# Kernel optimization log

Measured on AMD Instinct MI355X. Metric: run time of the kernel, lower is better.

## Reference

```python
import jax, jax.numpy as jnp
import numpy as np
import math

B, S, D, H, L, DF = 16, 512, 512, 8, 6, 2048
DK = D // H
EPS = 1e-6


def _xavier(key, shape):
    # xavier_uniform over the last two dims (matches nn.init.xavier_uniform_)
    fan_in, fan_out = shape[-2], shape[-1]
    lim = math.sqrt(6.0 / (fan_in + fan_out))
    return jax.random.uniform(key, shape, jnp.float32, -lim, lim)


def setup_inputs() -> dict:
    key = jax.random.key(0)
    ks = jax.random.split(key, 12)
    return {
        "x": jax.random.normal(ks[0], (B, S, D), jnp.float32),
        "pe_table": jax.random.normal(ks[1], (S, D), jnp.float32),  # _4by8_pe weight
        "pe_q_w": _xavier(ks[2], (D, D)), "pe_q_b": jnp.zeros((D,), jnp.float32),
        "pe_k_w": _xavier(ks[3], (D, D)), "pe_k_b": jnp.zeros((D,), jnp.float32),
        "Wq": _xavier(ks[4], (L, D, D)), "bq": jnp.zeros((L, D), jnp.float32),
        "Wk": _xavier(ks[5], (L, D, D)), "bk": jnp.zeros((L, D), jnp.float32),
        "Wv": _xavier(ks[6], (L, D, D)), "bv": jnp.zeros((L, D), jnp.float32),
        "Wo": _xavier(ks[7], (L, D, D)), "bo": jnp.zeros((L, D), jnp.float32),
        "ln1_g": jnp.ones((L, D), jnp.float32), "ln1_b": jnp.zeros((L, D), jnp.float32),
        "W1": _xavier(ks[8], (L, D, DF)), "b1": jnp.zeros((L, DF), jnp.float32),
        "W2": _xavier(ks[9], (L, DF, D)), "b2": jnp.zeros((L, D), jnp.float32),
        "ln2_g": jnp.ones((L, D), jnp.float32), "ln2_b": jnp.zeros((L, D), jnp.float32),
    }


def _layernorm(y, g, b):
    m = jnp.mean(y, axis=-1, keepdims=True)
    v = jnp.var(y, axis=-1, keepdims=True)  # biased, as torch LayerNorm
    return (y - m) * jax.lax.rsqrt(v + EPS) * g + b


def reference(x, pe_table, pe_q_w, pe_q_b, pe_k_w, pe_k_b,
              Wq, bq, Wk, bk, Wv, bv, Wo, bo,
              ln1_g, ln1_b, W1, b1, W2, b2, ln2_g, ln2_b):
    scale = math.sqrt(2 * DK)
    h = x * math.sqrt(D)

    # scores_pe is identical for every batch element (pe_onehot = arange repeated)
    pq = (pe_table @ pe_q_w + pe_q_b).reshape(S, H, DK).transpose(1, 0, 2)  # [H,S,dk]
    pk = (pe_table @ pe_k_w + pe_k_b).reshape(S, H, DK).transpose(1, 0, 2)  # [H,S,dk]
    scores_pe = jnp.einsum('hqd,hkd->hqk', pq, pk) / scale  # [H,S,S]

    def step(h, p):
        wq, bq_, wk, bk_, wv, bv_, wo, bo_, g1, gb1, w1, fb1, w2, fb2, g2, gb2 = p
        q = (h @ wq + bq_).reshape(B, S, H, DK).transpose(0, 2, 1, 3)  # [B,H,S,dk]
        k = (h @ wk + bk_).reshape(B, S, H, DK).transpose(0, 2, 1, 3)
        v = (h @ wv + bv_).reshape(B, S, H, DK).transpose(0, 2, 1, 3)
        scores = jnp.einsum('bhqd,bhkd->bhqk', q, k) / scale + scores_pe  # [B,H,S,S]
        attn = jax.nn.softmax(scores, axis=-1)
        o = jnp.einsum('bhqk,bhkd->bhqd', attn, v).transpose(0, 2, 1, 3).reshape(B, S, D)
        o = o @ wo + bo_
        h1 = _layernorm(o + h, g1, gb1)
        f = jax.nn.gelu(h1 @ w1 + fb1, approximate=False) @ w2 + fb2
        h2 = _layernorm(f + h1, g2, gb2)
        return h2, None

    params = (Wq, bq, Wk, bk, Wv, bv, Wo, bo, ln1_g, ln1_b, W1, b1, W2, b2, ln2_g, ln2_b)
    h, _ = jax.lax.scan(step, h, params)
    pe_out = jnp.broadcast_to(pe_table, (B, S, D))
    return h, pe_out
```

## Files before the change

kernel.cpp:

```cpp
#include <hip/hip_runtime.h>
#include <hip/hip_bf16.h>

typedef __hip_bfloat16 bf16;
typedef short bf16x8 __attribute__((ext_vector_type(8)));
typedef float f32x4 __attribute__((ext_vector_type(4)));

#define DEV static __device__ __forceinline__

DEV f32x4 fzero4(){ f32x4 z; z[0]=0.f; z[1]=0.f; z[2]=0.f; z[3]=0.f; return z; }

DEV void gl2lds16(const bf16* g, bf16* l){
  __builtin_amdgcn_global_load_lds(
    (const __attribute__((address_space(1))) void*)g,
    (__attribute__((address_space(3))) void*)l, 16, 0, 0);
}

enum { EP_F32=0, EP_BF16=1, EP_GELU=2, EP_HILO=3, EP_QKV=4 };

template<int EPI, int NMT>
__global__ __launch_bounds__(256) void gemm_bt(
    const bf16* A0, const bf16* A1, const bf16* A2,
    const bf16* B0, const bf16* B1, const bf16* B2,
    int npass, int lda, int ldb, int M, int N, int K,
    const float* __restrict__ bs0, const float* __restrict__ bs1, const float* __restrict__ bs2,
    float alpha, void* o0, void* o1, void* o2,
    int azs, int bzs, int ozs)
{
  constexpr int BM = NMT*32;
  __shared__ __align__(16) bf16 As[BM*32];
  __shared__ __align__(16) bf16 Bs[128*32];
  const int t = threadIdx.x;
  const int lane = t & 63;
  const int w = t >> 6;
  const int wr = w >> 1, wc = w & 1;
  const int m0 = blockIdx.y * BM, n0 = blockIdx.x * 128;
  const int l15 = lane & 15, l4 = lane >> 4;
  const int grow = (lane >> 2);
  const int gcol = (lane & 3) * 8;
  const int z = blockIdx.z;
  if (azs){ A0 += (size_t)z*azs; if(A1) A1 += (size_t)z*azs; if(A2) A2 += (size_t)z*azs; }
  if (bzs){ B0 += (size_t)z*bzs; if(B1) B1 += (size_t)z*bzs; if(B2) B2 += (size_t)z*bzs; }

  f32x4 acc[NMT][4];
  #pragma unroll
  for (int i=0;i<NMT;i++)
    #pragma unroll
    for (int j=0;j<4;j++) acc[i][j] = fzero4();

  for (int p=0;p<npass;p++){
    const bf16* Ag = (p==0) ? A0 : ((p==1) ? A1 : A2);
    const bf16* Bg = (p==0) ? B0 : ((p==1) ? B1 : B2);
    for (int k0=0;k0<K;k0+=32){
      if constexpr (NMT==4){
        #pragma unroll
        for (int q=0;q<2;q++){
          int row = w*32 + q*16 + grow;
          gl2lds16(Ag + (size_t)(m0+row)*lda + k0 + gcol, As + (w*32+q*16)*32);
          gl2lds16(Bg + (size_t)(n0+row)*ldb + k0 + gcol, Bs + (w*32+q*16)*32);
        }
      } else {
        int rA = w*16 + grow;
        gl2lds16(Ag + (size_t)(m0+rA)*lda + k0 + gcol, As + w*16*32);
        #pragma unroll
        for (int sb=0;sb<2;sb++){
          int rB = (2*w+sb)*16 + grow;
          gl2lds16(Bg + (size_t)(n0+rB)*ldb + k0 + gcol, Bs + (2*w+sb)*16*32);
        }
      }
      __syncthreads();
      bf16x8 af[NMT], bfv[4];
      #pragma unroll
      for (int mt=0;mt<NMT;mt++) af[mt] = *(const bf16x8*)(As + (wr*(NMT*16)+mt*16+l15)*32 + 8*l4);
      #pragma unroll
      for (int nt=0;nt<4;nt++) bfv[nt] = *(const bf16x8*)(Bs + (wc*64+nt*16+l15)*32 + 8*l4);
      #pragma unroll
      for (int mt=0;mt<NMT;mt++)
        #pragma unroll
        for (int nt=0;nt<4;nt++)
          acc[mt][nt] = __builtin_amdgcn_mfma_f32_16x16x32_bf16(af[mt], bfv[nt], acc[mt][nt], 0, 0, 0);
      __syncthreads();
    }
  }

  #pragma unroll
  for (int mt=0;mt<NMT;mt++){
    #pragma unroll
    for (int nt=0;nt<4;nt++){
      const int crow = m0 + wr*(NMT*16) + mt*16 + l4*4;
      const int ccol = n0 + wc*64 + nt*16 + l15;
      #pragma unroll
      for (int j=0;j<4;j++){
        float v = acc[mt][nt][j];
        int r = crow + j;
        if (EPI==EP_F32){
          float b = bs0 ? bs0[ccol] : 0.f;
          ((float*)o0)[(size_t)r*N + ccol] = alpha*v + b;
        } else if (EPI==EP_BF16){
          float b = bs0 ? bs0[ccol] : 0.f;
          ((bf16*)o0 + (size_t)z*ozs)[(size_t)r*N + ccol] = __float2bfloat16(alpha*v + b);
        } else if (EPI==EP_GELU){
          float xx = v + bs0[ccol];
          float g = 0.5f*xx*(1.f + erff(xx*0.70710678118654752f));
          ((bf16*)o0)[(size_t)r*N + ccol] = __float2bfloat16(g);
        } else if (EPI==EP_HILO){
          float xx = v + bs0[ccol];
          bf16 hi = __float2bfloat16(xx);
          ((bf16*)o0)[(size_t)r*N + ccol] = hi;
          ((bf16*)o1)[(size_t)r*N + ccol] = __float2bfloat16(xx - __bfloat162float(hi));
        } else {
          int n = ccol;
          if (n < 512){
            ((bf16*)o0)[(size_t)r*512 + n] = __float2bfloat16(v + bs0[n]);
          } else if (n < 1024){
            ((bf16*)o1)[(size_t)r*512 + (n-512)] = __float2bfloat16(v + bs1[n-512]);
          } else {
            int d = n - 1024;
            int bb = r >> 9, s = r & 511;
            int hh = d >> 6, dd = d & 63;
            ((bf16*)o2)[(size_t)(((bb*8)+hh)*64 + dd)*512 + s] = __float2bfloat16(v + bs2[d]);
          }
        }
      }
    }
  }
}

template<int SPLIT>
__global__ __launch_bounds__(256) void attn_mfma(
  const bf16* __restrict__ Q, const bf16* __restrict__ Qlo,
  const bf16* __restrict__ Kh, const bf16* __restrict__ Klo,
  const bf16* __restrict__ VT, const bf16* __restrict__ SPE,
  bf16* __restrict__ O)
{
  __shared__ __align__(16) bf16 K_lds[64*64];
  __shared__ __align__(16) bf16 V_lds[64*64];
  __shared__ __align__(16) bf16 Klo_lds[SPLIT ? 64*64 : 8];
  __shared__ __align__(16) bf16 P_lds[4][16*64];
  const int t = threadIdx.x;
  const int lane = t & 63, w = t >> 6;
  const int l15 = lane & 15, l4 = lane >> 4;
  const int bid = blockIdx.x;
  const int h = bid & 7;
  const int s2 = bid >> 3;
  const int b = s2 >> 3, qblk = s2 & 7;
  const int q0 = qblk*64 + w*16;
  const float inv_scale = 0.08838834764831845f;
  const int xorv = (l15 & 7) << 3;

  bf16x8 qf[2], qflo[2];
  #pragma unroll
  for (int kst=0;kst<2;kst++){
    qf[kst] = *(const bf16x8*)(Q + (size_t)(b*512 + q0 + l15)*512 + h*64 + kst*32 + 8*l4);
    if (SPLIT) qflo[kst] = *(const bf16x8*)(Qlo + (size_t)(b*512 + q0 + l15)*512 + h*64 + kst*32 + 8*l4);
  }
  f32x4 accO[4];
  #pragma unroll
  for (int dt=0;dt<4;dt++) accO[dt] = fzero4();
  float mrow[4], lrow[4];
  #pragma unroll
  for (int j=0;j<4;j++){ mrow[j] = -1e30f; lrow[j] = 0.f; }

  const bf16* spe_h = SPE + (size_t)h*262144;
  const bf16* vbase = VT + (size_t)((b*8)+h)*32768;

  for (int n0=0;n0<512;n0+=64){
    #pragma unroll
    for (int st=0;st<2;st++){
      int rl = w*16 + st*8 + (lane>>3);
      int jj = (lane&7) ^ (rl&7);
      gl2lds16(Kh + (size_t)(b*512 + n0 + rl)*512 + h*64 + jj*8, K_lds + (w*16+st*8)*64);
      if (SPLIT)
        gl2lds16(Klo + (size_t)(b*512 + n0 + rl)*512 + h*64 + jj*8, Klo_lds + (w*16+st*8)*64);
      gl2lds16(vbase + (size_t)rl*512 + n0 + jj*8, V_lds + (w*16+st*8)*64);
    }
    __syncthreads();

    f32x4 sc[4];
    #pragma unroll
    for (int c=0;c<4;c++) sc[c] = fzero4();
    #pragma unroll
    for (int c=0;c<4;c++){
      const int rr = c*16 + l15;
      #pragma unroll
      for (int kst=0;kst<2;kst++){
        bf16x8 kf = *(const bf16x8*)(K_lds + rr*64 + ((kst*32 + 8*l4) ^ xorv));
        sc[c] = __builtin_amdgcn_mfma_f32_16x16x32_bf16(qf[kst], kf, sc[c], 0,0,0);
        if (SPLIT){
          sc[c] = __builtin_amdgcn_mfma_f32_16x16x32_bf16(qflo[kst], kf, sc[c], 0,0,0);
          bf16x8 kfl = *(const bf16x8*)(Klo_lds + rr*64 + ((kst*32 + 8*l4) ^ xorv));
          sc[c] = __builtin_amdgcn_mfma_f32_16x16x32_bf16(qf[kst], kfl, sc[c], 0,0,0);
        }
      }
    }
    float sv[4][4];
    #pragma unroll
    for (int c=0;c<4;c++)
      #pragma unroll
      for (int j=0;j<4;j++){
        int qr = q0 + l4*4 + j;
        sv[c][j] = sc[c][j]*inv_scale + __bfloat162float(spe_h[(size_t)qr*512 + n0 + c*16 + l15]);
      }
    float fac[4];
    #pragma unroll
    for (int j=0;j<4;j++){
      float m2 = fmaxf(fmaxf(sv[0][j],sv[1][j]), fmaxf(sv[2][j],sv[3][j]));
      m2 = fmaxf(m2, __shfl_xor(m2,1));
      m2 = fmaxf(m2, __shfl_xor(m2,2));
      m2 = fmaxf(m2, __shfl_xor(m2,4));
      m2 = fmaxf(m2, __shfl_xor(m2,8));
      float mn = fmaxf(mrow[j], m2);
      fac[j] = __expf(mrow[j] - mn);
      mrow[j] = mn;
    }
    #pragma unroll
    for (int j=0;j<4;j++){
      int row = l4*4 + j;
      float ts = 0.f;
      #pragma unroll
      for (int c=0;c<4;c++){
        float pv = __expf(sv[c][j] - mrow[j]);
        ts += pv;
        P_lds[w][row*64 + ((c*16 + l15) ^ ((row&7)<<3))] = __float2bfloat16(pv);
      }
      ts += __shfl_xor(ts,1); ts += __shfl_xor(ts,2);
      ts += __shfl_xor(ts,4); ts += __shfl_xor(ts,8);
      lrow[j] = lrow[j]*fac[j] + ts;
      #pragma unroll
      for (int dt=0;dt<4;dt++) accO[dt][j] *= fac[j];
    }
    #pragma unroll
    for (int kv=0;kv<2;kv++){
      bf16x8 pf = *(const bf16x8*)(P_lds[w] + l15*64 + ((kv*32 + 8*l4) ^ xorv));
      #pragma unroll
      for (int dt=0;dt<4;dt++){
        const int d = dt*16 + l15;
        bf16x8 vf = *(const bf16x8*)(V_lds + d*64 + ((kv*32 + 8*l4) ^ xorv));
        accO[dt] = __builtin_amdgcn_mfma_f32_16x16x32_bf16(pf, vf, accO[dt], 0,0,0);
      }
    }
    __syncthreads();
  }
  #pragma unroll
  for (int dt=0;dt<4;dt++)
    #pragma unroll
    for (int j=0;j<4;j++){
      float v = accO[dt][j] / lrow[j];
      int r = q0 + l4*4 + j;
      O[(size_t)(b*512+r)*512 + h*64 + dt*16 + l15] = __float2bfloat16(v);
    }
}

__global__ __launch_bounds__(256) void ln_kernel(
  const float* __restrict__ tmp, const float* __restrict__ resid,
  const float* __restrict__ g, const float* __restrict__ bta,
  float* __restrict__ outf, bf16* __restrict__ outb)
{
  const int row = blockIdx.x*4 + (threadIdx.x>>6);
  const int lane = threadIdx.x & 63;
  const size_t base = (size_t)row*512 + lane*8;
  float4 a0 = *(const float4*)(tmp+base),   a1 = *(const float4*)(tmp+base+4);
  float4 r0 = *(const float4*)(resid+base), r1 = *(const float4*)(resid+base+4);
  float x[8];
  x[0]=a0.x+r0.x; x[1]=a0.y+r0.y; x[2]=a0.z+r0.z; x[3]=a0.w+r0.w;
  x[4]=a1.x+r1.x; x[5]=a1.y+r1.y; x[6]=a1.z+r1.z; x[7]=a1.w+r1.w;
  float s=0.f, sq=0.f;
  #pragma unroll
  for (int i=0;i<8;i++){ s += x[i]; sq += x[i]*x[i]; }
  #pragma unroll
  for (int d=1; d<64; d<<=1){ s += __shfl_xor(s,d); sq += __shfl_xor(sq,d); }
  float mean = s*(1.f/512.f);
  float var = sq*(1.f/512.f) - mean*mean;
  float rr = rsqrtf(var + 1e-6f);
  #pragma unroll
  for (int i=0;i<8;i++){
    int d = lane*8 + i;
    float y = (x[i]-mean)*rr*g[d] + bta[d];
    outf[base+i] = y;
    outb[base+i] = __float2bfloat16(y);
  }
}

template<bool LO>
__global__ __launch_bounds__(256) void tcast(
  const float* __restrict__ src, int srcStride,
  bf16* __restrict__ dst, int dstStride, bf16* __restrict__ dlo,
  int R, int C)
{
  __shared__ float tile[32][33];
  const int z = blockIdx.z;
  src += (size_t)z*srcStride;
  dst += (size_t)z*dstStride;
  const int tx = threadIdx.x & 31, ty = threadIdx.x >> 5;
  const int r0 = blockIdx.y*32, c0 = blockIdx.x*32;
  #pragma unroll
  for (int p=0;p<4;p++)
    tile[ty+8*p][tx] = src[(size_t)(r0+ty+8*p)*C + c0+tx];
  __syncthreads();
  #pragma unroll
  for (int p=0;p<4;p++){
    float v = tile[tx][ty+8*p];
    bf16 hi = __float2bfloat16(v);
    dst[(size_t)(c0+ty+8*p)*R + r0+tx] = hi;
    if (LO) dlo[(size_t)(c0+ty+8*p)*R + r0+tx] = __float2bfloat16(v - __bfloat162float(hi));
  }
}

__global__ void castbf(const float* __restrict__ in, bf16* __restrict__ out, int n){
  int i = blockIdx.x*blockDim.x + threadIdx.x;
  if (i < n) out[i] = __float2bfloat16(in[i]);
}

__global__ void init_h(const float* __restrict__ x, float* __restrict__ hf,
                       bf16* __restrict__ hb, bf16* __restrict__ hlo, int n){
  int i = blockIdx.x*blockDim.x + threadIdx.x;
  if (i < n){
    float v = x[i]*22.627416997969522f;
    hf[i] = v;
    bf16 hi = __float2bfloat16(v);
    hb[i] = hi;
    hlo[i] = __float2bfloat16(v - __bfloat162float(hi));
  }
}

__global__ void write_out(const float* __restrict__ hf, const float* __restrict__ pe,
                          float* __restrict__ out, int n1){
  int i = blockIdx.x*blockDim.x + threadIdx.x;
  if (i < n1){
    out[i] = hf[i];
    out[n1 + i] = pe[i & 262143];
  }
}

extern "C" void kernel_launch(void* const* d_in, const int* in_sizes, int n_in,
                              void* d_out, int out_size, void* d_ws, size_t ws_size,
                              hipStream_t stream)
{
  const float* x    = (const float*)d_in[0];
  const float* pe   = (const float*)d_in[1];
  const float* peqw = (const float*)d_in[2];
  const float* peqb = (const float*)d_in[3];
  const float* pekw = (const float*)d_in[4];
  const float* pekb = (const float*)d_in[5];
  const float* Wq   = (const float*)d_in[6];
  const float* bq   = (const float*)d_in[7];
  const float* Wk   = (const float*)d_in[8];
  const float* bk   = (const float*)d_in[9];
  const float* Wv   = (const float*)d_in[10];
  const float* bv   = (const float*)d_in[11];
  const float* Wo   = (const float*)d_in[12];
  const float* bo   = (const float*)d_in[13];
  const float* g1   = (const float*)d_in[14];
  const float* bb1  = (const float*)d_in[15];
  const float* W1   = (const float*)d_in[16];
  const float* fb1  = (const float*)d_in[17];
  const float* W2   = (const float*)d_in[18];
  const float* fb2  = (const float*)d_in[19];
  const float* g2   = (const float*)d_in[20];
  const float* bb2  = (const float*)d_in[21];

  char* wp = (char*)d_ws;
  auto carve = [&](size_t bytes)->void*{ void* r = (void*)wp; wp += (bytes + 255) & ~(size_t)255; return r; };
  float* hf   = (float*)carve(16777216);
  float* h1f  = (float*)carve(16777216);
  char*  regB = (char*)carve(16777216);
  float* tmp  = (float*)regB;
  bf16*  qlo  = (bf16*)regB;
  bf16*  klo  = (bf16*)(regB + 8388608);
  bf16* hb    = (bf16*)carve(8388608);
  bf16* hlo   = (bf16*)carve(8388608);
  bf16* h1b   = (bf16*)carve(8388608);
  char* regA  = (char*)carve(33554432);
  bf16* gbuf  = (bf16*)regA;
  bf16* qb    = (bf16*)regA;
  bf16* kbuf  = (bf16*)(regA + 8388608);
  bf16* vT    = (bf16*)(regA + 16777216);
  bf16* obuf  = (bf16*)(regA + 25165824);
  bf16* WqkvT = (bf16*)carve(9437184);
  bf16* WoT   = (bf16*)carve(3145728);
  bf16* W1T   = (bf16*)carve(12582912);
  bf16* W2T   = (bf16*)carve(12582912);
  bf16* Wq0h  = (bf16*)carve(524288);
  bf16* Wq0l  = (bf16*)carve(524288);
  bf16* Wk0h  = (bf16*)carve(524288);
  bf16* Wk0l  = (bf16*)carve(524288);
  bf16* peb   = (bf16*)carve(524288);
  bf16* pqwT  = (bf16*)carve(524288);
  bf16* pkwT  = (bf16*)carve(524288);
  bf16* pqb   = (bf16*)carve(524288);
  bf16* pkb   = (bf16*)carve(524288);
  bf16* spe   = (bf16*)carve(4194304);

  dim3 B256(256);
  const float INV_SCALE = 0.08838834764831845f;

  tcast<false><<<dim3(16,16,6),B256,0,stream>>>(Wq, 262144, WqkvT,          786432, nullptr, 512, 512);
  tcast<false><<<dim3(16,16,6),B256,0,stream>>>(Wk, 262144, WqkvT + 262144, 786432, nullptr, 512, 512);
  tcast<false><<<dim3(16,16,6),B256,0,stream>>>(Wv, 262144, WqkvT + 524288, 786432, nullptr, 512, 512);
  tcast<false><<<dim3(16,16,6),B256,0,stream>>>(Wo, 262144, WoT, 262144, nullptr, 512, 512);
  tcast<false><<<dim3(64,16,6),B256,0,stream>>>(W1, 1048576, W1T, 1048576, nullptr, 512, 2048);
  tcast<false><<<dim3(16,64,6),B256,0,stream>>>(W2, 1048576, W2T, 1048576, nullptr, 2048, 512);
  tcast<false><<<dim3(16,16,1),B256,0,stream>>>(peqw, 262144, pqwT, 262144, nullptr, 512, 512);
  tcast<false><<<dim3(16,16,1),B256,0,stream>>>(pekw, 262144, pkwT, 262144, nullptr, 512, 512);
  tcast<true ><<<dim3(16,16,1),B256,0,stream>>>(Wq, 262144, Wq0h, 262144, Wq0l, 512, 512);
  tcast<true ><<<dim3(16,16,1),B256,0,stream>>>(Wk, 262144, Wk0h, 262144, Wk0l, 512, 512);
  castbf<<<1024,B256,0,stream>>>(pe, peb, 262144);
  init_h<<<16384,B256,0,stream>>>(x, hf, hb, hlo, 4194304);

  gemm_bt<EP_BF16,2><<<dim3(4,8),B256,0,stream>>>(peb,nullptr,nullptr, pqwT,nullptr,nullptr, 1, 512,512, 512,512,512, peqb,nullptr,nullptr, 1.f, pqb,nullptr,nullptr, 0,0,0);
  gemm_bt<EP_BF16,2><<<dim3(4,8),B256,0,stream>>>(peb,nullptr,nullptr, pkwT,nullptr,nullptr, 1, 512,512, 512,512,512, pekb,nullptr,nullptr, 1.f, pkb,nullptr,nullptr, 0,0,0);
  gemm_bt<EP_BF16,2><<<dim3(4,8,8),B256,0,stream>>>(pqb,nullptr,nullptr, pkb,nullptr,nullptr, 1, 512,512, 512,512,64, nullptr,nullptr,nullptr, INV_SCALE, spe,nullptr,nullptr, 64,64,262144);

  for (int l=0;l<6;l++){
    const bf16* WQKV = WqkvT + l*786432;
    const float* bql = bq + l*512;
    const float* bkl = bk + l*512;
    const float* bvl = bv + l*512;
    gemm_bt<EP_QKV,4><<<dim3(12,64),B256,0,stream>>>(hb,nullptr,nullptr, WQKV,nullptr,nullptr, 1, 512,512, 8192,1536,512, bql,bkl,bvl, 1.f, qb, kbuf, vT, 0,0,0);
    if (l==0){
      gemm_bt<EP_HILO,2><<<dim3(4,128),B256,0,stream>>>(hb,hb,hlo, Wq0h,Wq0l,Wq0h, 3, 512,512, 8192,512,512, bql,nullptr,nullptr, 1.f, qb, qlo, nullptr, 0,0,0);
      gemm_bt<EP_HILO,2><<<dim3(4,128),B256,0,stream>>>(hb,hb,hlo, Wk0h,Wk0l,Wk0h, 3, 512,512, 8192,512,512, bkl,nullptr,nullptr, 1.f, kbuf, klo, nullptr, 0,0,0);
      attn_mfma<1><<<dim3(1024),B256,0,stream>>>(qb,qlo,kbuf,klo,vT,spe,obuf);
    } else {
      attn_mfma<0><<<dim3(1024),B256,0,stream>>>(qb,qb,kbuf,kbuf,vT,spe,obuf);
    }
    gemm_bt<EP_F32,2><<<dim3(4,128),B256,0,stream>>>(obuf,nullptr,nullptr, WoT+l*262144,nullptr,nullptr, 1, 512,512, 8192,512,512, bo+l*512,nullptr,nullptr, 1.f, tmp,nullptr,nullptr, 0,0,0);
    ln_kernel<<<2048,B256,0,stream>>>(tmp, hf, g1+l*512, bb1+l*512, h1f, h1b);
    gemm_bt<EP_GELU,4><<<dim3(16,64),B256,0,stream>>>(h1b,nullptr,nullptr, W1T+l*1048576,nullptr,nullptr, 1, 512,512, 8192,2048,512, fb1+l*2048,nullptr,nullptr, 1.f, gbuf,nullptr,nullptr, 0,0,0);
    gemm_bt<EP_F32,2><<<dim3(4,128),B256,0,stream>>>(gbuf,nullptr,nullptr, W2T+l*1048576,nullptr,nullptr, 1, 2048,2048, 8192,512,2048, fb2+l*512,nullptr,nullptr, 1.f, tmp,nullptr,nullptr, 0,0,0);
    ln_kernel<<<2048,B256,0,stream>>>(tmp, h1f, g2+l*512, bb2+l*512, hf, hb);
  }
  write_out<<<16384,B256,0,stream>>>(hf, pe, (float*)d_out, 4194304);
}
```

Baseline: 1.271 ms.

## Double-buffer GEMM LDS tiles, XCD-aware block mapping, wider attention KV tiles

The GEMM now keeps two LDS buffers and issues the next K-slice's global-to-LDS loads right after the barrier, before computing on the current slice. This aims to overlap loads with MFMA and drops one barrier per iteration. Blocks are remapped from a 1D grid so that each XCD (bid&7) works on a contiguous chunk of M rows, to improve L2 reuse. The attention kernel now processes 128 keys per iteration instead of 64, halving the number of barriers and online-softmax rescale steps, at the cost of more LDS and registers. The single barrier per step may be unsafe: a fast wave can start staging the next tile into the buffer that slower waves are still reading.

```diff
diff --git a/kernel.cpp b/kernel.cpp
--- a/kernel.cpp
+++ b/kernel.cpp
@@ -24,16 +24,22 @@
     int npass, int lda, int ldb, int M, int N, int K,
     const float* __restrict__ bs0, const float* __restrict__ bs1, const float* __restrict__ bs2,
     float alpha, void* o0, void* o1, void* o2,
-    int azs, int bzs, int ozs)
+    int nn, int mchunk, int azs, int bzs, int ozs)
 {
   constexpr int BM = NMT*32;
-  __shared__ __align__(16) bf16 As[BM*32];
-  __shared__ __align__(16) bf16 Bs[128*32];
+  __shared__ __align__(16) bf16 As[2][BM*32];
+  __shared__ __align__(16) bf16 Bs[2][128*32];
   const int t = threadIdx.x;
   const int lane = t & 63;
   const int w = t >> 6;
   const int wr = w >> 1, wc = w & 1;
-  const int m0 = blockIdx.y * BM, n0 = blockIdx.x * 128;
+  const int bid = blockIdx.x;
+  const int xcd = bid & 7;
+  const int idx = bid >> 3;
+  const int qm = idx / nn;
+  const int mb = xcd*mchunk + qm;
+  const int nb = idx - qm*nn;
+  const int m0 = mb*BM, n0 = nb*128;
   const int l15 = lane & 15, l4 = lane >> 4;
   const int grow = (lane >> 2);
   const int gcol = (lane & 3) * 8;
@@ -41,44 +47,53 @@
   if (azs){ A0 += (size_t)z*azs; if(A1) A1 += (size_t)z*azs; if(A2) A2 += (size_t)z*azs; }
   if (bzs){ B0 += (size_t)z*bzs; if(B1) B1 += (size_t)z*bzs; if(B2) B2 += (size_t)z*bzs; }
 
+  auto Aof = [&](int p){ return (p==0)?A0:((p==1)?A1:A2); };
+  auto Bof = [&](int p){ return (p==0)?B0:((p==1)?B1:B2); };
+
+  auto stageAB = [&](int cb, const bf16* Ag, const bf16* Bg, int k0){
+    if constexpr (NMT==4){
+      #pragma unroll
+      for (int q=0;q<2;q++){
+        int row = w*32 + q*16 + grow;
+        gl2lds16(Ag + (size_t)(m0+row)*lda + k0 + gcol, As[cb] + (w*32+q*16)*32);
+        gl2lds16(Bg + (size_t)(n0+row)*ldb + k0 + gcol, Bs[cb] + (w*32+q*16)*32);
+      }
+    } else {
+      int rA = w*16 + grow;
+      gl2lds16(Ag + (size_t)(m0+rA)*lda + k0 + gcol, As[cb] + w*16*32);
+      #pragma unroll
+      for (int sb=0;sb<2;sb++){
+        int rB = (2*w+sb)*16 + grow;
+        gl2lds16(Bg + (size_t)(n0+rB)*ldb + k0 + gcol, Bs[cb] + (2*w+sb)*16*32);
+      }
+    }
+  };
+
   f32x4 acc[NMT][4];
   #pragma unroll
   for (int i=0;i<NMT;i++)
     #pragma unroll
     for (int j=0;j<4;j++) acc[i][j] = fzero4();
 
+  int cur = 0;
+  stageAB(0, A0, B0, 0);
   for (int p=0;p<npass;p++){
-    const bf16* Ag = (p==0) ? A0 : ((p==1) ? A1 : A2);
-    const bf16* Bg = (p==0) ? B0 : ((p==1) ? B1 : B2);
     for (int k0=0;k0<K;k0+=32){
-      if constexpr (NMT==4){
-        #pragma unroll
-        for (int q=0;q<2;q++){
-          int row = w*32 + q*16 + grow;
-          gl2lds16(Ag + (size_t)(m0+row)*lda + k0 + gcol, As + (w*32+q*16)*32);
-          gl2lds16(Bg + (size_t)(n0+row)*ldb + k0 + gcol, Bs + (w*32+q*16)*32);
-        }
-      } else {
-        int rA = w*16 + grow;
-        gl2lds16(Ag + (size_t)(m0+rA)*lda + k0 + gcol, As + w*16*32);
-        #pragma unroll
-        for (int sb=0;sb<2;sb++){
-          int rB = (2*w+sb)*16 + grow;
-          gl2lds16(Bg + (size_t)(n0+rB)*ldb + k0 + gcol, Bs + (2*w+sb)*16*32);
-        }
-      }
       __syncthreads();
+      int kn = k0 + 32;
+      if (kn < K)            stageAB(cur^1, Aof(p), Bof(p), kn);
+      else if (p+1 < npass)  stageAB(cur^1, Aof(p+1), Bof(p+1), 0);
       bf16x8 af[NMT], bfv[4];
       #pragma unroll
-      for (int mt=0;mt<NMT;mt++) af[mt] = *(const bf16x8*)(As + (wr*(NMT*16)+mt*16+l15)*32 + 8*l4);
-      #pragma unroll
-      for (int nt=0;nt<4;nt++) bfv[nt] = *(const bf16x8*)(Bs + (wc*64+nt*16+l15)*32 + 8*l4);
+      for (int mt=0;mt<NMT;mt++) af[mt] = *(const bf16x8*)(As[cur] + (wr*(NMT*16)+mt*16+l15)*32 + 8*l4);
+      #pragma unroll
+      for (int nt=0;nt<4;nt++) bfv[nt] = *(const bf16x8*)(Bs[cur] + (wc*64+nt*16+l15)*32 + 8*l4);
       #pragma unroll
       for (int mt=0;mt<NMT;mt++)
         #pragma unroll
         for (int nt=0;nt<4;nt++)
           acc[mt][nt] = __builtin_amdgcn_mfma_f32_16x16x32_bf16(af[mt], bfv[nt], acc[mt][nt], 0, 0, 0);
-      __syncthreads();
+      cur ^= 1;
     }
   }
 
@@ -132,10 +147,10 @@
   const bf16* __restrict__ VT, const bf16* __restrict__ SPE,
   bf16* __restrict__ O)
 {
-  __shared__ __align__(16) bf16 K_lds[64*64];
-  __shared__ __align__(16) bf16 V_lds[64*64];
-  __shared__ __align__(16) bf16 Klo_lds[SPLIT ? 64*64 : 8];
-  __shared__ __align__(16) bf16 P_lds[4][16*64];
+  __shared__ __align__(16) bf16 K_lds[128*64];
+  __shared__ __align__(16) bf16 V_lds[64*128];
+  __shared__ __align__(16) bf16 Klo_lds[SPLIT ? 128*64 : 8];
+  __shared__ __align__(16) bf16 P_lds[4][16*128];
   const int t = threadIdx.x;
   const int lane = t & 63, w = t >> 6;
   const int l15 = lane & 15, l4 = lane >> 4;
@@ -163,23 +178,28 @@
   const bf16* spe_h = SPE + (size_t)h*262144;
   const bf16* vbase = VT + (size_t)((b*8)+h)*32768;
 
-  for (int n0=0;n0<512;n0+=64){
-    #pragma unroll
-    for (int st=0;st<2;st++){
-      int rl = w*16 + st*8 + (lane>>3);
+  for (int n0=0;n0<512;n0+=128){
+    #pragma unroll
+    for (int st=0;st<4;st++){
+      int rl = w*32 + st*8 + (lane>>3);
       int jj = (lane&7) ^ (rl&7);
-      gl2lds16(Kh + (size_t)(b*512 + n0 + rl)*512 + h*64 + jj*8, K_lds + (w*16+st*8)*64);
+      gl2lds16(Kh + (size_t)(b*512 + n0 + rl)*512 + h*64 + jj*8, K_lds + (w*32+st*8)*64);
       if (SPLIT)
-        gl2lds16(Klo + (size_t)(b*512 + n0 + rl)*512 + h*64 + jj*8, Klo_lds + (w*16+st*8)*64);
-      gl2lds16(vbase + (size_t)rl*512 + n0 + jj*8, V_lds + (w*16+st*8)*64);
+        gl2lds16(Klo + (size_t)(b*512 + n0 + rl)*512 + h*64 + jj*8, Klo_lds + (w*32+st*8)*64);
+    }
+    #pragma unroll
+    for (int st=0;st<4;st++){
+      int d = w*16 + st*4 + (lane>>4);
+      int jj = (lane&15) ^ (d&7);
+      gl2lds16(vbase + (size_t)d*512 + n0 + jj*8, V_lds + (w*16+st*4)*128);
     }
     __syncthreads();
 
-    f32x4 sc[4];
-    #pragma unroll
-    for (int c=0;c<4;c++) sc[c] = fzero4();
-    #pragma unroll
-    for (int c=0;c<4;c++){
+    f32x4 sc[8];
+    #pragma unroll
+    for (int c=0;c<8;c++) sc[c] = fzero4();
+    #pragma unroll
+    for (int c=0;c<8;c++){
       const int rr = c*16 + l15;
       #pragma unroll
       for (int kst=0;kst<2;kst++){
@@ -192,9 +212,9 @@
         }
       }
     }
-    float sv[4][4];
-    #pragma unroll
-    for (int c=0;c<4;c++)
+    float sv[8][4];
+    #pragma unroll
+    for (int c=0;c<8;c++)
       #pragma unroll
       for (int j=0;j<4;j++){
         int qr = q0 + l4*4 + j;
@@ -203,7 +223,9 @@
     float fac[4];
     #pragma unroll
     for (int j=0;j<4;j++){
-      float m2 = fmaxf(fmaxf(sv[0][j],sv[1][j]), fmaxf(sv[2][j],sv[3][j]));
+      float m2 = -1e30f;
+      #pragma unroll
+      for (int c=0;c<8;c++) m2 = fmaxf(m2, sv[c][j]);
       m2 = fmaxf(m2, __shfl_xor(m2,1));
       m2 = fmaxf(m2, __shfl_xor(m2,2));
       m2 = fmaxf(m2, __shfl_xor(m2,4));
@@ -217,10 +239,10 @@
       int row = l4*4 + j;
       float ts = 0.f;
       #pragma unroll
-      for (int c=0;c<4;c++){
+      for (int c=0;c<8;c++){
         float pv = __expf(sv[c][j] - mrow[j]);
         ts += pv;
-        P_lds[w][row*64 + ((c*16 + l15) ^ ((row&7)<<3))] = __float2bfloat16(pv);
+        P_lds[w][row*128 + ((c*16 + l15) ^ ((row&7)<<3))] = __float2bfloat16(pv);
       }
       ts += __shfl_xor(ts,1); ts += __shfl_xor(ts,2);
       ts += __shfl_xor(ts,4); ts += __shfl_xor(ts,8);
@@ -229,12 +251,12 @@
       for (int dt=0;dt<4;dt++) accO[dt][j] *= fac[j];
     }
     #pragma unroll
-    for (int kv=0;kv<2;kv++){
-      bf16x8 pf = *(const bf16x8*)(P_lds[w] + l15*64 + ((kv*32 + 8*l4) ^ xorv));
+    for (int kv=0;kv<4;kv++){
+      bf16x8 pf = *(const bf16x8*)(P_lds[w] + l15*128 + ((kv*32 + 8*l4) ^ xorv));
       #pragma unroll
       for (int dt=0;dt<4;dt++){
         const int d = dt*16 + l15;
-        bf16x8 vf = *(const bf16x8*)(V_lds + d*64 + ((kv*32 + 8*l4) ^ xorv));
+        bf16x8 vf = *(const bf16x8*)(V_lds + d*128 + ((kv*32 + 8*l4) ^ xorv));
         accO[dt] = __builtin_amdgcn_mfma_f32_16x16x32_bf16(pf, vf, accO[dt], 0,0,0);
       }
     }
@@ -406,27 +428,27 @@
   castbf<<<1024,B256,0,stream>>>(pe, peb, 262144);
   init_h<<<16384,B256,0,stream>>>(x, hf, hb, hlo, 4194304);
 
-  gemm_bt<EP_BF16,2><<<dim3(4,8),B256,0,stream>>>(peb,nullptr,nullptr, pqwT,nullptr,nullptr, 1, 512,512, 512,512,512, peqb,nullptr,nullptr, 1.f, pqb,nullptr,nullptr, 0,0,0);
-  gemm_bt<EP_BF16,2><<<dim3(4,8),B256,0,stream>>>(peb,nullptr,nullptr, pkwT,nullptr,nullptr, 1, 512,512, 512,512,512, pekb,nullptr,nullptr, 1.f, pkb,nullptr,nullptr, 0,0,0);
-  gemm_bt<EP_BF16,2><<<dim3(4,8,8),B256,0,stream>>>(pqb,nullptr,nullptr, pkb,nullptr,nullptr, 1, 512,512, 512,512,64, nullptr,nullptr,nullptr, INV_SCALE, spe,nullptr,nullptr, 64,64,262144);
+  gemm_bt<EP_BF16,2><<<dim3(32),B256,0,stream>>>(peb,nullptr,nullptr, pqwT,nullptr,nullptr, 1, 512,512, 512,512,512, peqb,nullptr,nullptr, 1.f, pqb,nullptr,nullptr, 4,1, 0,0,0);
+  gemm_bt<EP_BF16,2><<<dim3(32),B256,0,stream>>>(peb,nullptr,nullptr, pkwT,nullptr,nullptr, 1, 512,512, 512,512,512, pekb,nullptr,nullptr, 1.f, pkb,nullptr,nullptr, 4,1, 0,0,0);
+  gemm_bt<EP_BF16,2><<<dim3(32,1,8),B256,0,stream>>>(pqb,nullptr,nullptr, pkb,nullptr,nullptr, 1, 512,512, 512,512,64, nullptr,nullptr,nullptr, INV_SCALE, spe,nullptr,nullptr, 4,1, 64,64,262144);
 
   for (int l=0;l<6;l++){
     const bf16* WQKV = WqkvT + l*786432;
     const float* bql = bq + l*512;
     const float* bkl = bk + l*512;
     const float* bvl = bv + l*512;
-    gemm_bt<EP_QKV,4><<<dim3(12,64),B256,0,stream>>>(hb,nullptr,nullptr, WQKV,nullptr,nullptr, 1, 512,512, 8192,1536,512, bql,bkl,bvl, 1.f, qb, kbuf, vT, 0,0,0);
+    gemm_bt<EP_QKV,4><<<dim3(768),B256,0,stream>>>(hb,nullptr,nullptr, WQKV,nullptr,nullptr, 1, 512,512, 8192,1536,512, bql,bkl,bvl, 1.f, qb, kbuf, vT, 12,8, 0,0,0);
     if (l==0){
-      gemm_bt<EP_HILO,2><<<dim3(4,128),B256,0,stream>>>(hb,hb,hlo, Wq0h,Wq0l,Wq0h, 3, 512,512, 8192,512,512, bql,nullptr,nullptr, 1.f, qb, qlo, nullptr, 0,0,0);
-      gemm_bt<EP_HILO,2><<<dim3(4,128),B256,0,stream>>>(hb,hb,hlo, Wk0h,Wk0l,Wk0h, 3, 512,512, 8192,512,512, bkl,nullptr,nullptr, 1.f, kbuf, klo, nullptr, 0,0,0);
+      gemm_bt<EP_HILO,2><<<dim3(512),B256,0,stream>>>(hb,hb,hlo, Wq0h,Wq0l,Wq0h, 3, 512,512, 8192,512,512, bql,nullptr,nullptr, 1.f, qb, qlo, nullptr, 4,16, 0,0,0);
+      gemm_bt<EP_HILO,2><<<dim3(512),B256,0,stream>>>(hb,hb,hlo, Wk0h,Wk0l,Wk0h, 3, 512,512, 8192,512,512, bkl,nullptr,nullptr, 1.f, kbuf, klo, nullptr, 4,16, 0,0,0);
       attn_mfma<1><<<dim3(1024),B256,0,stream>>>(qb,qlo,kbuf,klo,vT,spe,obuf);
     } else {
       attn_mfma<0><<<dim3(1024),B256,0,stream>>>(qb,qb,kbuf,kbuf,vT,spe,obuf);
     }
-    gemm_bt<EP_F32,2><<<dim3(4,128),B256,0,stream>>>(obuf,nullptr,nullptr, WoT+l*262144,nullptr,nullptr, 1, 512,512, 8192,512,512, bo+l*512,nullptr,nullptr, 1.f, tmp,nullptr,nullptr, 0,0,0);
+    gemm_bt<EP_F32,2><<<dim3(512),B256,0,stream>>>(obuf,nullptr,nullptr, WoT+l*262144,nullptr,nullptr, 1, 512,512, 8192,512,512, bo+l*512,nullptr,nullptr, 1.f, tmp,nullptr,nullptr, 4,16, 0,0,0);
     ln_kernel<<<2048,B256,0,stream>>>(tmp, hf, g1+l*512, bb1+l*512, h1f, h1b);
-    gemm_bt<EP_GELU,4><<<dim3(16,64),B256,0,stream>>>(h1b,nullptr,nullptr, W1T+l*1048576,nullptr,nullptr, 1, 512,512, 8192,2048,512, fb1+l*2048,nullptr,nullptr, 1.f, gbuf,nullptr,nullptr, 0,0,0);
-    gemm_bt<EP_F32,2><<<dim3(4,128),B256,0,stream>>>(gbuf,nullptr,nullptr, W2T+l*1048576,nullptr,nullptr, 1, 2048,2048, 8192,512,2048, fb2+l*512,nullptr,nullptr, 1.f, tmp,nullptr,nullptr, 0,0,0);
+    gemm_bt<EP_GELU,4><<<dim3(1024),B256,0,stream>>>(h1b,nullptr,nullptr, W1T+l*1048576,nullptr,nullptr, 1, 512,512, 8192,2048,512, fb1+l*2048,nullptr,nullptr, 1.f, gbuf,nullptr,nullptr, 16,8, 0,0,0);
+    gemm_bt<EP_F32,2><<<dim3(512),B256,0,stream>>>(gbuf,nullptr,nullptr, W2T+l*1048576,nullptr,nullptr, 1, 2048,2048, 8192,512,2048, fb2+l*512,nullptr,nullptr, 1.f, tmp,nullptr,nullptr, 4,16, 0,0,0);
     ln_kernel<<<2048,B256,0,stream>>>(tmp, h1f, g2+l*512, bb2+l*512, hf, hb);
   }
   write_out<<<16384,B256,0,stream>>>(hf, pe, (float*)d_out, 4194304);
```

Result: slower. 1.311 ms (+3.2%).
